# Performance work log

Measured on AMD Instinct MI355X. Metric: run time of the kernel, lower is better.

The kernel has to match this reference:

```python
import jax, jax.numpy as jnp
import numpy as np

N_HEAD = 16


def setup_inputs() -> dict:
    key = jax.random.key(0)
    ks = jax.random.split(key, 5)
    B, T, C = 4, 4096, 2048
    H = N_HEAD
    x = jax.random.normal(ks[0], (B, T, C), dtype=jnp.float32)
    # torch Linear weights are (out_features, in_features); bias=False
    Wa = jax.random.normal(ks[1], (C, C), dtype=jnp.float32) * 0.02
    Wp = jax.random.normal(ks[2], (C, C), dtype=jnp.float32) * 0.02
    temp = jnp.ones((H, 1), dtype=jnp.float32)
    denom_bias = jnp.zeros((H, T, 1), dtype=jnp.float32)  # block_size == T
    return {"x": x, "Wa": Wa, "Wp": Wp, "temp": temp, "denom_bias": denom_bias}


def reference(x, Wa, Wp, temp, denom_bias):
    B, T, C = x.shape
    H = N_HEAD
    D = C // H
    # c_attn (no bias): y = x @ Wa^T
    w = jnp.einsum('btc,oc->bto', x, Wa)
    w = w.reshape(B, T, H, D).transpose(0, 2, 1, 3)  # (B,H,T,D)
    w_sq = w * w
    # running second-moment denominator along time
    denom = jnp.maximum(jnp.cumsum(w_sq, axis=2), 1e-12)
    w_normed = w_sq / denom + denom_bias[:, :T, :]          # (B,H,T,D)
    tmp = jnp.sum(w_normed, axis=-1) * temp                 # (B,H,T), temp (H,1) broadcasts
    Pi = jax.nn.softmax(tmp, axis=1)                        # softmax over heads
    # token-statistics attention: running Pi-weighted mean of w_sq
    dots = jnp.cumsum(w_sq * Pi[..., None], axis=2) / (jnp.cumsum(Pi, axis=-1) + 1e-8)[..., None]
    attn = 1.0 / (1.0 + dots)                               # (B,H,T,D)
    y = -(w * Pi[..., None]) * attn                         # (B,H,T,D)
    y = y.transpose(0, 2, 1, 3).reshape(B, T, C)
    # c_proj (no bias)
    y = jnp.einsum('btc,oc->bto', y, Wp)
    return y
```

## Files before the change

### kernel.cpp

```cpp
#include <hip/hip_runtime.h>
#include <hip/hip_bf16.h>
#include <stdint.h>

#define BB 4
#define TT 4096
#define CC 2048
#define HH 16
#define DD 128
#define MM (BB*TT)
#define KK CC
#define NNx CC
#define NTP 16

#define NCH 128
#define CHL (TT/NCH)

typedef unsigned short u16;
typedef unsigned int   u32;
typedef __bf16 bf16x8 __attribute__((ext_vector_type(8)));
typedef float  f32x4  __attribute__((ext_vector_type(4)));

__device__ __forceinline__ float bf2f(u32 lo) {
  union { u32 u; float f; } z; z.u = lo << 16; return z.f;
}
__device__ __forceinline__ u16 f2bf(float f) {
  union { float f; u32 u; } z; z.f = f;
  u32 u = z.u;
  return (u16)((u + 0x7FFFu + ((u >> 16) & 1u)) >> 16);
}
__device__ __forceinline__ void unpack8(uint4 v, float* a) {
  a[0]=bf2f(v.x&0xffffu); a[1]=bf2f(v.x>>16);
  a[2]=bf2f(v.y&0xffffu); a[3]=bf2f(v.y>>16);
  a[4]=bf2f(v.z&0xffffu); a[5]=bf2f(v.z>>16);
  a[6]=bf2f(v.w&0xffffu); a[7]=bf2f(v.w>>16);
}

__global__ void cvt3(const float* __restrict__ x, const float* __restrict__ wa,
                     const float* __restrict__ wp, u16* __restrict__ ox,
                     u16* __restrict__ oa, u16* __restrict__ op) {
  const long nx = (long)MM * KK;
  const long nw = (long)CC * CC;
  long i = ((long)blockIdx.x * blockDim.x + threadIdx.x) * 8;
  const float* in; u16* out; long j;
  if (i < nx)            { in = x;  out = ox; j = i; }
  else if (i < nx + nw)  { in = wa; out = oa; j = i - nx; }
  else                   { in = wp; out = op; j = i - nx - nw; }
  float4 v0 = *(const float4*)(in + j);
  float4 v1 = *(const float4*)(in + j + 4);
  uint4 o;
  o.x = (u32)f2bf(v0.x) | ((u32)f2bf(v0.y) << 16);
  o.y = (u32)f2bf(v0.z) | ((u32)f2bf(v0.w) << 16);
  o.z = (u32)f2bf(v1.x) | ((u32)f2bf(v1.y) << 16);
  o.w = (u32)f2bf(v1.z) | ((u32)f2bf(v1.w) << 16);
  *(uint4*)(out + j) = o;
}

__device__ __forceinline__ void gload16(const void* g, void* l) {
  __builtin_amdgcn_global_load_lds(
      (__attribute__((address_space(1))) void*)g,
      (__attribute__((address_space(3))) void*)l, 16, 0, 0);
}

template<int OUTF32, int EPI>
__global__ __launch_bounds__(512, 2)
void gemm256(const u16* __restrict__ A, const u16* __restrict__ Bm,
             float* __restrict__ Cf, u16* __restrict__ Cb,
             float* __restrict__ S1)
{
  __shared__ u16 As[4][8192];
  __shared__ u16 Bs[4][8192];
  const int tid  = threadIdx.x;
  const int wid  = tid >> 6;
  const int lane = tid & 63;
  const int wm = wid >> 2, wn = wid & 3;
  const int fr = lane & 15, kg = lane >> 4;
  const int orig = blockIdx.x;
  const int nid  = ((orig & 7) << 6) | (orig >> 3);
  const int m0 = (nid >> 3) * 256;
  const int n0 = (nid & 7) * 256;

  const int srow = tid >> 2;
  const int sc   = (tid & 3) ^ ((srow >> 1) & 3);
  const u16* gA0 = A  + (size_t)(m0 + srow) * KK + sc * 8;
  const u16* gA1 = gA0 + (size_t)128 * KK;
  const u16* gB0 = Bm + (size_t)(n0 + srow) * KK + sc * 8;
  const u16* gB1 = gB0 + (size_t)128 * KK;
  const int ldst0 = wid * 512;
  const int ldst1 = 4096 + wid * 512;

  const int cs    = kg ^ ((fr >> 1) & 3);
  const int abase = (wm * 128 + fr) * 32 + cs * 8;
  const int bbase = (wn * 64  + fr) * 32 + cs * 8;

  f32x4 acc[8][4];
  #pragma unroll
  for (int i = 0; i < 8; ++i)
    #pragma unroll
    for (int j = 0; j < 4; ++j) acc[i][j] = (f32x4){0.f,0.f,0.f,0.f};

  auto stA = [&](int slot, int ko) {
    ko = (ko < KK) ? ko : 0;
    gload16(gA0 + ko, &As[slot][ldst0]);
    gload16(gA1 + ko, &As[slot][ldst1]);
  };
  auto stB = [&](int slot, int ko) {
    ko = (ko < KK) ? ko : 0;
    gload16(gB0 + ko, &Bs[slot][ldst0]);
    gload16(gB1 + ko, &Bs[slot][ldst1]);
  };

  stA(0, 0);  stB(0, 0);
  stA(1, 32); stB(1, 32);
  stA(2, 64); stB(2, 64);
  asm volatile("s_waitcnt vmcnt(8)" ::: "memory");
  __builtin_amdgcn_s_barrier();

  bf16x8 av[4], bv[4];

#define PH(CSLOT, MH, LOADB, STMT, DOWAIT) do {                               \
    _Pragma("unroll")                                                         \
    for (int f = 0; f < 4; ++f)                                               \
      av[f] = *(const bf16x8*)&As[CSLOT][abase + ((MH)*64 + f*16)*32];        \
    if (LOADB) {                                                              \
      _Pragma("unroll")                                                       \
      for (int f = 0; f < 4; ++f)                                             \
        bv[f] = *(const bf16x8*)&Bs[CSLOT][bbase + f*16*32];                  \
    }                                                                         \
    STMT;                                                                     \
    if (DOWAIT) asm volatile("s_waitcnt vmcnt(8)" ::: "memory");              \
    __builtin_amdgcn_s_barrier();                                             \
    __builtin_amdgcn_s_setprio(1);                                            \
    _Pragma("unroll")                                                         \
    for (int f = 0; f < 4; ++f)                                               \
      _Pragma("unroll")                                                       \
      for (int n = 0; n < 4; ++n)                                             \
        acc[(MH)*4+f][n] = __builtin_amdgcn_mfma_f32_16x16x32_bf16(          \
            av[f], bv[n], acc[(MH)*4+f][n], 0, 0, 0);                         \
    __builtin_amdgcn_s_setprio(0);                                            \
    __builtin_amdgcn_s_barrier();                                             \
  } while (0)

  for (int it = 0; it < NTP; ++it) {
    const int kb = it * 128;
    PH(0, 0, 1, stA(3, kb + 96), 0);
    PH(0, 1, 0, stB(3, kb + 96), 1);
    PH(1, 0, 1, stA(0, kb + 128), 0);
    PH(1, 1, 0, stB(0, kb + 128), 1);
    PH(2, 0, 1, stA(1, kb + 160), 0);
    PH(2, 1, 0, stB(1, kb + 160), 1);
    PH(3, 0, 1, stA(2, kb + 192), 0);
    PH(3, 1, 0, stB(2, kb + 192), 1);
  }
#undef PH

  const int row0 = m0 + wm * 128 + kg * 4;
  const int col0 = n0 + wn * 64 + fr;
  if (OUTF32) {
    #pragma unroll
    for (int mf = 0; mf < 8; ++mf)
      #pragma unroll
      for (int nf = 0; nf < 4; ++nf)
        #pragma unroll
        for (int r = 0; r < 4; ++r)
          Cf[(size_t)(row0 + mf*16 + r) * NNx + col0 + nf*16] = acc[mf][nf][r];
  } else {
    float csum[4][4];
    #pragma unroll
    for (int p = 0; p < 4; ++p)
      #pragma unroll
      for (int nf = 0; nf < 4; ++nf) csum[p][nf] = 0.f;
    #pragma unroll
    for (int mf = 0; mf < 8; ++mf)
      #pragma unroll
      for (int nf = 0; nf < 4; ++nf)
        #pragma unroll
        for (int r = 0; r < 4; ++r) {
          u16 hb = f2bf(acc[mf][nf][r]);
          Cb[(size_t)(row0 + mf*16 + r) * NNx + col0 + nf*16] = hb;
          if (EPI) { float av_ = bf2f(hb); csum[mf>>1][nf] += av_ * av_; }
        }
    if (EPI) {
      const int b   = m0 >> 12;
      const int ch0 = ((m0 & (TT-1)) >> 5) + wm * 4;
      #pragma unroll
      for (int p = 0; p < 4; ++p)
        #pragma unroll
        for (int nf = 0; nf < 4; ++nf) {
          float v = csum[p][nf];
          v += __shfl_xor(v, 16, 64);
          v += __shfl_xor(v, 32, 64);
          if (kg == 0)
            S1[(size_t)(ch0 + p) * (BB*CC) + b * CC + col0 + nf*16] = v;
        }
    }
  }
}

template<int S>
__global__ __launch_bounds__(256)
void excl_scan_wave(float* __restrict__ p, int ncol) {
  const int w = (int)((blockIdx.x * 256 + threadIdx.x) >> 6);
  const int l = threadIdx.x & 63;
  if (w >= ncol) return;
  float a = p[(size_t)l * S + w];
  float b = p[(size_t)(64 + l) * S + w];
  float ia = a, ib = b;
  #pragma unroll
  for (int off = 1; off < 64; off <<= 1) {
    float ta = __shfl_up(ia, off, 64);
    float tb = __shfl_up(ib, off, 64);
    if (l >= off) { ia += ta; ib += tb; }
  }
  float totA = __shfl(ia, 63, 64);
  p[(size_t)l * S + w]        = ia - a;
  p[(size_t)(64 + l) * S + w] = totA + ib - b;
}

__global__ __launch_bounds__(256)
void pass_c(const u16* __restrict__ w, float* __restrict__ S,
            float* __restrict__ SP, float* __restrict__ Pi,
            const float* __restrict__ temp, const float* __restrict__ dbias)
{
  __shared__ float sm[2][HH];
  const int ch = blockIdx.x, b = blockIdx.y;
  const int tid = threadIdx.x;
  const int h = tid >> 4;
  const int t0 = ch * CHL;
  const u16* wrow = w + ((size_t)b*TT + t0) * CC + tid*8;
  float* Srow = S + (size_t)ch * (BB*CC) + b * CC + tid*8;
  float c0[8], s2[8];
  #pragma unroll
  for (int j = 0; j < 8; ++j) { c0[j] = Srow[j]; s2[j] = 0.f; }
  const float th = temp[h];
  const float* db = dbias + (size_t)h * TT + t0;
  float sp = 0.f;
  uint4 v = *(const uint4*)wrow;
  for (int t = 0; t < CHL; ++t) {
    uint4 vn = v;
    if (t + 1 < CHL) vn = *(const uint4*)(wrow + (size_t)(t+1) * CC);
    float a2[8];
    { float a[8]; unpack8(v, a);
      #pragma unroll
      for (int j = 0; j < 8; ++j) a2[j] = a[j]*a[j]; }
    float val = 0.f;
    #pragma unroll
    for (int j = 0; j < 8; ++j) {
      c0[j] += a2[j];
      val += a2[j] * __builtin_amdgcn_rcpf(fmaxf(c0[j], 1e-12f));
    }
    val += __shfl_xor(val, 1, 64);
    val += __shfl_xor(val, 2, 64);
    val += __shfl_xor(val, 4, 64);
    val += __shfl_xor(val, 8, 64);
    const float tmp = th * (val + (float)DD * db[t]);
    if ((tid & 15) == 0) sm[t & 1][h] = tmp;
    __syncthreads();
    float m = -1e30f;
    #pragma unroll
    for (int hh = 0; hh < HH; ++hh) m = fmaxf(m, sm[t & 1][hh]);
    float ssum = 0.f;
    #pragma unroll
    for (int hh = 0; hh < HH; ++hh) ssum += __expf(sm[t & 1][hh] - m);
    const float pi = __expf(sm[t & 1][h] - m) * __builtin_amdgcn_rcpf(ssum);
    sp += pi;
    #pragma unroll
    for (int j = 0; j < 8; ++j) s2[j] += a2[j] * pi;
    if ((tid & 15) == 0) Pi[((size_t)b*TT + t0 + t) * HH + h] = pi;
    v = vn;
  }
  #pragma unroll
  for (int j = 0; j < 8; ++j) Srow[j] = s2[j];
  if ((tid & 15) == 0) SP[ch * (BB*HH) + b * HH + h] = sp;
}

__global__ __launch_bounds__(256)
void pass_d(const u16* __restrict__ w, const float* __restrict__ S2,
            const float* __restrict__ SP, const float* __restrict__ Pi,
            u16* __restrict__ ymid)
{
  const int ch = blockIdx.x, b = blockIdx.y;
  const int tid = threadIdx.x;
  const int h = tid >> 4;
  const int t0 = ch * CHL;
  const u16* wrow = w + ((size_t)b*TT + t0) * CC + tid*8;
  u16* yrow = ymid + ((size_t)b*TT + t0) * CC + tid*8;
  const float* Srow = S2 + (size_t)ch * (BB*CC) + b * CC + tid*8;
  float c2[8];
  #pragma unroll
  for (int j = 0; j < 8; ++j) c2[j] = Srow[j];
  float cp = SP[ch * (BB*HH) + b * HH + h];
  const float* prow = Pi + ((size_t)b*TT + t0) * HH + h;
  uint4 v = *(const uint4*)wrow;
  for (int t = 0; t < CHL; ++t) {
    uint4 vn = v;
    if (t + 1 < CHL) vn = *(const uint4*)(wrow + (size_t)(t+1) * CC);
    const float pi = prow[(size_t)t * HH];
    cp += pi;
    const float invp = __builtin_amdgcn_rcpf(cp + 1e-8f);
    float a[8]; unpack8(v, a);
    float y[8];
    #pragma unroll
    for (int j = 0; j < 8; ++j) {
      const float a2 = a[j]*a[j];
      c2[j] += a2 * pi;
      const float d = c2[j] * invp;
      y[j] = -(a[j] * pi) * __builtin_amdgcn_rcpf(1.f + d);
    }
    uint4 o;
    o.x = (u32)f2bf(y[0]) | ((u32)f2bf(y[1]) << 16);
    o.y = (u32)f2bf(y[2]) | ((u32)f2bf(y[3]) << 16);
    o.z = (u32)f2bf(y[4]) | ((u32)f2bf(y[5]) << 16);
    o.w = (u32)f2bf(y[6]) | ((u32)f2bf(y[7]) << 16);
    *(uint4*)(yrow + (size_t)t * CC) = o;
    v = vn;
  }
}

extern "C" void kernel_launch(void* const* d_in, const int* in_sizes, int n_in,
                              void* d_out, int out_size, void* d_ws, size_t ws_size,
                              hipStream_t stream) {
  const float* x     = (const float*)d_in[0];
  const float* Wa    = (const float*)d_in[1];
  const float* Wp    = (const float*)d_in[2];
  const float* temp  = (const float*)d_in[3];
  const float* dbias = (const float*)d_in[4];
  float* out = (float*)d_out;

  char* ws = (char*)d_ws;
  u16*  xb   = (u16*)(ws);
  u16*  Wab  = (u16*)(ws + 67108864);
  u16*  Wpb  = (u16*)(ws + 75497472);
  u16*  wbuf = (u16*)(ws + 83886080);
  float* S1  = (float*)(ws + 150994944);
  float* SP  = (float*)(ws + 155189248);
  float* Pi  = (float*)(ws + 67108864);
  u16*  ymid = xb;

  cvt3<<<20480, 256, 0, stream>>>(x, Wa, Wp, xb, Wab, Wpb);

  gemm256<0,1><<<512, 512, 0, stream>>>(xb, Wab, nullptr, wbuf, S1);

  excl_scan_wave<BB*CC><<<2048, 256, 0, stream>>>(S1, BB*CC);

  dim3 gc(NCH, BB);
  pass_c<<<gc, 256, 0, stream>>>(wbuf, S1, SP, Pi, temp, dbias);

  excl_scan_wave<BB*CC><<<2048, 256, 0, stream>>>(S1, BB*CC);
  excl_scan_wave<BB*HH><<<16, 256, 0, stream>>>(SP, BB*HH);

  pass_d<<<gc, 256, 0, stream>>>(wbuf, S1, SP, Pi, ymid);

  gemm256<1,0><<<512, 512, 0, stream>>>(ymid, Wpb, out, nullptr, nullptr);
}
```

Before: 402.5 us.

## Batch two timesteps per barrier in pass_c and use LDS-tiled column scans

The pass_c loop now handles two timesteps per iteration with a double-buffered shared array, so each 256-thread block hits one __syncthreads per two timesteps instead of one per timestep. The exclusive column scans change from a wave-shuffle scan over strided column reads to a kernel that loads a 128-column tile into LDS with coalesced row reads, scans serially per column, and writes it back. The scan now runs only 64 blocks with a long serial loop per thread, which may limit parallelism.

```diff
diff --git a/kernel.cpp b/kernel.cpp
--- a/kernel.cpp
+++ b/kernel.cpp
@@ -196,24 +196,35 @@
   }
 }
 
-template<int S>
 __global__ __launch_bounds__(256)
-void excl_scan_wave(float* __restrict__ p, int ncol) {
-  const int w = (int)((blockIdx.x * 256 + threadIdx.x) >> 6);
-  const int l = threadIdx.x & 63;
-  if (w >= ncol) return;
-  float a = p[(size_t)l * S + w];
-  float b = p[(size_t)(64 + l) * S + w];
-  float ia = a, ib = b;
-  #pragma unroll
-  for (int off = 1; off < 64; off <<= 1) {
-    float ta = __shfl_up(ia, off, 64);
-    float tb = __shfl_up(ib, off, 64);
-    if (l >= off) { ia += ta; ib += tb; }
-  }
-  float totA = __shfl(ia, 63, 64);
-  p[(size_t)l * S + w]        = ia - a;
-  p[(size_t)(64 + l) * S + w] = totA + ib - b;
+void excl_lds(float* __restrict__ p, int stride, int ncol) {
+  __shared__ float tile[NCH][128];
+  const int c0 = blockIdx.x * 128;
+  const int tid = threadIdx.x;
+  const int half = tid >> 7;
+  const int cc = tid & 127;
+  const bool ok = (c0 + cc) < ncol;
+  #pragma unroll 4
+  for (int r = 0; r < NCH; r += 2) {
+    const int row = r + half;
+    if (ok) tile[row][cc] = p[(size_t)row * stride + c0 + cc];
+  }
+  __syncthreads();
+  if (tid < 128) {
+    float run = 0.f;
+    #pragma unroll
+    for (int r = 0; r < NCH; ++r) {
+      float v = tile[r][tid];
+      tile[r][tid] = run;
+      run += v;
+    }
+  }
+  __syncthreads();
+  #pragma unroll 4
+  for (int r = 0; r < NCH; r += 2) {
+    const int row = r + half;
+    if (ok) p[(size_t)row * stride + c0 + cc] = tile[row][cc];
+  }
 }
 
 __global__ __launch_bounds__(256)
@@ -221,7 +232,7 @@
             float* __restrict__ SP, float* __restrict__ Pi,
             const float* __restrict__ temp, const float* __restrict__ dbias)
 {
-  __shared__ float sm[2][HH];
+  __shared__ float sm[2][2][HH];
   const int ch = blockIdx.x, b = blockIdx.y;
   const int tid = threadIdx.x;
   const int h = tid >> 4;
@@ -234,39 +245,61 @@
   const float th = temp[h];
   const float* db = dbias + (size_t)h * TT + t0;
   float sp = 0.f;
-  uint4 v = *(const uint4*)wrow;
-  for (int t = 0; t < CHL; ++t) {
-    uint4 vn = v;
-    if (t + 1 < CHL) vn = *(const uint4*)(wrow + (size_t)(t+1) * CC);
-    float a2[8];
-    { float a[8]; unpack8(v, a);
-      #pragma unroll
-      for (int j = 0; j < 8; ++j) a2[j] = a[j]*a[j]; }
-    float val = 0.f;
-    #pragma unroll
-    for (int j = 0; j < 8; ++j) {
-      c0[j] += a2[j];
-      val += a2[j] * __builtin_amdgcn_rcpf(fmaxf(c0[j], 1e-12f));
-    }
-    val += __shfl_xor(val, 1, 64);
-    val += __shfl_xor(val, 2, 64);
-    val += __shfl_xor(val, 4, 64);
-    val += __shfl_xor(val, 8, 64);
-    const float tmp = th * (val + (float)DD * db[t]);
-    if ((tid & 15) == 0) sm[t & 1][h] = tmp;
+  uint4 v0 = *(const uint4*)wrow;
+  uint4 v1 = *(const uint4*)(wrow + (size_t)CC);
+  for (int tp = 0; tp < CHL; tp += 2) {
+    const int pb = (tp >> 1) & 1;
+    uint4 n0, n1;
+    if (tp + 2 < CHL) {
+      n0 = *(const uint4*)(wrow + (size_t)(tp+2) * CC);
+      n1 = *(const uint4*)(wrow + (size_t)(tp+3) * CC);
+    } else { n0 = v0; n1 = v1; }
+    float a20[8], a21[8];
+    { float a[8]; unpack8(v0, a);
+      float val = 0.f;
+      #pragma unroll
+      for (int j = 0; j < 8; ++j) {
+        a20[j] = a[j]*a[j];
+        c0[j] += a20[j];
+        val += a20[j] * __builtin_amdgcn_rcpf(fmaxf(c0[j], 1e-12f));
+      }
+      val += __shfl_xor(val, 1, 64);
+      val += __shfl_xor(val, 2, 64);
+      val += __shfl_xor(val, 4, 64);
+      val += __shfl_xor(val, 8, 64);
+      if ((tid & 15) == 0) sm[pb][0][h] = th * (val + (float)DD * db[tp]);
+    }
+    { float a[8]; unpack8(v1, a);
+      float val = 0.f;
+      #pragma unroll
+      for (int j = 0; j < 8; ++j) {
+        a21[j] = a[j]*a[j];
+        c0[j] += a21[j];
+        val += a21[j] * __builtin_amdgcn_rcpf(fmaxf(c0[j], 1e-12f));
+      }
+      val += __shfl_xor(val, 1, 64);
+      val += __shfl_xor(val, 2, 64);
+      val += __shfl_xor(val, 4, 64);
+      val += __shfl_xor(val, 8, 64);
+      if ((tid & 15) == 0) sm[pb][1][h] = th * (val + (float)DD * db[tp+1]);
+    }
     __syncthreads();
-    float m = -1e30f;
-    #pragma unroll
-    for (int hh = 0; hh < HH; ++hh) m = fmaxf(m, sm[t & 1][hh]);
-    float ssum = 0.f;
-    #pragma unroll
-    for (int hh = 0; hh < HH; ++hh) ssum += __expf(sm[t & 1][hh] - m);
-    const float pi = __expf(sm[t & 1][h] - m) * __builtin_amdgcn_rcpf(ssum);
-    sp += pi;
-    #pragma unroll
-    for (int j = 0; j < 8; ++j) s2[j] += a2[j] * pi;
-    if ((tid & 15) == 0) Pi[((size_t)b*TT + t0 + t) * HH + h] = pi;
-    v = vn;
+    #pragma unroll
+    for (int u = 0; u < 2; ++u) {
+      float m = -1e30f;
+      #pragma unroll
+      for (int hh = 0; hh < HH; ++hh) m = fmaxf(m, sm[pb][u][hh]);
+      float ssum = 0.f;
+      #pragma unroll
+      for (int hh = 0; hh < HH; ++hh) ssum += __expf(sm[pb][u][hh] - m);
+      const float pi = __expf(sm[pb][u][h] - m) * __builtin_amdgcn_rcpf(ssum);
+      sp += pi;
+      const float* a2 = u ? a21 : a20;
+      #pragma unroll
+      for (int j = 0; j < 8; ++j) s2[j] += a2[j] * pi;
+      if ((tid & 15) == 0) Pi[((size_t)b*TT + t0 + tp + u) * HH + h] = pi;
+    }
+    v0 = n0; v1 = n1;
   }
   #pragma unroll
   for (int j = 0; j < 8; ++j) Srow[j] = s2[j];
@@ -340,13 +373,13 @@
 
   gemm256<0,1><<<512, 512, 0, stream>>>(xb, Wab, nullptr, wbuf, S1);
 
-  excl_scan_wave<BB*CC><<<2048, 256, 0, stream>>>(S1, BB*CC);
+  excl_lds<<<64, 256, 0, stream>>>(S1, BB*CC, BB*CC);
 
   dim3 gc(NCH, BB);
   pass_c<<<gc, 256, 0, stream>>>(wbuf, S1, SP, Pi, temp, dbias);
 
-  excl_scan_wave<BB*CC><<<2048, 256, 0, stream>>>(S1, BB*CC);
-  excl_scan_wave<BB*HH><<<16, 256, 0, stream>>>(SP, BB*HH);
+  excl_lds<<<64, 256, 0, stream>>>(S1, BB*CC, BB*CC);
+  excl_lds<<<1, 256, 0, stream>>>(SP, BB*HH, BB*HH);
 
   pass_d<<<gc, 256, 0, stream>>>(wbuf, S1, SP, Pi, ymid);
 
```

Measured after the change: 402.5 us. Within noise of the previous version (+0.0%).
